# Optimization experiments

Hardware: AMD Instinct MI355X
Metric: run time of the kernel (lower is better)

Reference implementation:

```python
import jax, jax.numpy as jnp
import numpy as np

D_MODEL = 2048
N_HEADS = 16
HEAD_DIM = D_MODEL // N_HEADS  # 128
MAX_POS = 2048


def _precompute_cos_sin(max_pos, head_dim):
    inv_freq = 1.0 / (10000.0 ** (jnp.arange(0, head_dim, 2, dtype=jnp.float32) / head_dim))
    t = jnp.arange(max_pos, dtype=jnp.float32)
    freqs = jnp.outer(t, inv_freq)          # [max_pos, head_dim//2]
    emb = jnp.concatenate([freqs, freqs], axis=-1)  # [max_pos, head_dim]
    return jnp.cos(emb), jnp.sin(emb)


def _rotate_half(x):
    x1, x2 = x[..., : x.shape[-1] // 2], x[..., x.shape[-1] // 2 :]
    return jnp.concatenate([-x2, x1], axis=-1)


def setup_inputs() -> dict:
    key = jax.random.key(0)
    kx, kq, kk, kv, ko = jax.random.split(key, 5)
    B, S = 2, 2048
    x = jax.random.normal(kx, (B, S, D_MODEL), dtype=jnp.float32)
    scale = 1.0 / np.sqrt(D_MODEL)
    # torch Linear weights are [out_features, in_features]
    Wq = jax.random.normal(kq, (D_MODEL, D_MODEL), dtype=jnp.float32) * scale
    Wk = jax.random.normal(kk, (D_MODEL, D_MODEL), dtype=jnp.float32) * scale
    Wv = jax.random.normal(kv, (D_MODEL, D_MODEL), dtype=jnp.float32) * scale
    Wo = jax.random.normal(ko, (D_MODEL, D_MODEL), dtype=jnp.float32) * scale
    cos, sin = _precompute_cos_sin(MAX_POS, HEAD_DIM)
    # causal mask: True where attention is disallowed (masked_fill semantics)
    mask = jnp.triu(jnp.ones((S, S), dtype=bool), k=1)
    mask = jnp.broadcast_to(mask[None], (B, S, S))
    return {"x": x, "Wq": Wq, "Wk": Wk, "Wv": Wv, "Wo": Wo,
            "cos": cos, "sin": sin, "mask": mask}


def reference(x, Wq, Wk, Wv, Wo, cos, sin, mask):
    B, S, _ = x.shape
    H, Dh = N_HEADS, HEAD_DIM
    scaling = Dh ** -0.5

    def split_heads(y):  # [B,S,D] -> [B,H,S,Dh]
        return y.reshape(B, S, H, Dh).transpose(0, 2, 1, 3)

    q = split_heads(x @ Wq.T)
    k = split_heads(x @ Wk.T)
    v = split_heads(x @ Wv.T)

    c = cos[:S][None, None]  # [1,1,S,Dh]
    s = sin[:S][None, None]
    q = q * c + _rotate_half(q) * s
    k = k * c + _rotate_half(k) * s

    scores = jnp.einsum("bhqd,bhkd->bhqk", q, k) * scaling
    scores = jnp.where(mask[:, None], -jnp.inf, scores)
    attn = jax.nn.softmax(scores, axis=-1)
    out = jnp.einsum("bhqk,bhkd->bhqd", attn, v)  # [B,H,S,Dh]
    out = out.transpose(0, 2, 1, 3).reshape(B, S, H * Dh)
    return out @ Wo.T
```

## Files before the change

### kernel.cpp

```cpp
#include <hip/hip_runtime.h>

typedef float f32x4 __attribute__((ext_vector_type(4)));
typedef short s16x8 __attribute__((ext_vector_type(8)));
typedef unsigned short u16;
typedef u16 u16x4 __attribute__((ext_vector_type(4)));

#define SEQ 2048
#define BATCH 2
#define NH 16
#define DH 128
#define DM 2048
#define MROWS (BATCH * SEQ)

__device__ constexpr float SCALE2 = 0.12751879523531f;

__device__ __forceinline__ u16 f2bf(float f) {
  unsigned u = __float_as_uint(f);
  u += 0x7fffu + ((u >> 16) & 1u);
  return (u16)(u >> 16);
}
__device__ __forceinline__ float bf2f(u16 b) {
  return __uint_as_float(((unsigned)b) << 16);
}

__device__ __forceinline__ void gld_lds16(const void* g, void* l) {
  __builtin_amdgcn_global_load_lds(
      (const __attribute__((address_space(1))) unsigned int*)g,
      (__attribute__((address_space(3))) unsigned int*)l, 16, 0, 0);
}

__global__ __launch_bounds__(256) void cast_all(const float* __restrict__ x,
                                                const float* __restrict__ Wq,
                                                const float* __restrict__ Wk,
                                                const float* __restrict__ Wv,
                                                const float* __restrict__ Wo,
                                                u16* __restrict__ xb,
                                                u16* __restrict__ Wqkvb,
                                                u16* __restrict__ Wob) {
  long i = (long)blockIdx.x * 256 + threadIdx.x;
  const float* src;
  u16* dst;
  long off;
  if (i < 2097152)      { src = x;  dst = xb;              off = i; }
  else if (i < 3145728) { src = Wq; dst = Wqkvb;           off = i - 2097152; }
  else if (i < 4194304) { src = Wk; dst = Wqkvb + 4194304; off = i - 3145728; }
  else if (i < 5242880) { src = Wv; dst = Wqkvb + 8388608; off = i - 4194304; }
  else                  { src = Wo; dst = Wob;             off = i - 5242880; }
  float4 v = ((const float4*)src)[off];
  u16x4 o;
  o[0] = f2bf(v.x); o[1] = f2bf(v.y); o[2] = f2bf(v.z); o[3] = f2bf(v.w);
  ((u16x4*)dst)[off] = o;
}


#define BCOL(NF) (wn * 32 + ((NF) & 1) * 16 + ((NF) >> 1) * 64 + r)

#define GEMM_V3_BODY(A, B)                                                    \
  __shared__ u16 SMEM[49152];                                      \
  u16 (*Alds)[16384] = (u16(*)[16384])SMEM;                    \
  u16 (*Blds)[8192]  = (u16(*)[8192])(SMEM + 32768);           \
  const int tid = threadIdx.x, wave = tid >> 6, lane = tid & 63;              \
  const int r = lane & 15, g = lane >> 4;                                     \
  const int wm = wave >> 1, wn = wave & 1;                                    \
  const int bid = blockIdx.x;                                                 \
  const int swz = (bid & 7) * (gridDim.x >> 3) + (bid >> 3);                  \
  const int m0 = (swz & 15) * 256;                                            \
  const int n0 = (swz >> 4) * 128;                                            \
  const int lrow = lane >> 3;                                                 \
  const int csrc = (lane & 7) ^ lrow;                                         \
  f32x4 acc[4][4] = {};                                                       \
  s16x8 aF[2][4], bF[2][4];                                                   \
  STAGE_A(0, 0, 0); STAGE_B(0, 0, 0); STAGE_A(0, 1, 0); STAGE_B(0, 1, 0);     \
  STAGE_A(1, 0, 1); STAGE_B(1, 0, 1);                                         \
  asm volatile("s_waitcnt vmcnt(3)" ::: "memory");                            \
  __builtin_amdgcn_s_barrier();                                               \
  for (int t = 0; t < 32; ++t) {                                              \
    const int bt = t & 1, bn = bt ^ 1;                                        \
    const u16* Ab = Alds[bt];                                                 \
    const u16* Bb = Blds[bt];                                                 \
    READ_K(0);                                                                \
    __builtin_amdgcn_sched_barrier(0);                                        \
    READ_K(1);                                                                \
    if (t < 31) { STAGE_A(t + 1, 1, bn); STAGE_B(t + 1, 1, bn); }             \
    asm volatile("s_waitcnt lgkmcnt(8)" ::: "memory");                        \
    __builtin_amdgcn_sched_barrier(0);                                        \
    MFMA_K(0);                                                                \
    asm volatile("s_waitcnt lgkmcnt(0)" ::: "memory");                        \
    __builtin_amdgcn_sched_barrier(0);                                        \
    __builtin_amdgcn_s_barrier();                                             \
    if (t < 30) { STAGE_A(t + 2, 0, bt); STAGE_B(t + 2, 0, bt); }             \
    MFMA_K(1);                                                                \
    if (t < 30)       asm volatile("s_waitcnt vmcnt(3)" ::: "memory");        \
    else if (t == 30) asm volatile("s_waitcnt vmcnt(0)" ::: "memory");        \
    __builtin_amdgcn_s_barrier();                                             \
  }

#define STAGE_A(TA, MH, BUF) do {                                             \
  _Pragma("unroll") for (int i_ = 0; i_ < 2; ++i_) {                          \
    const int row0_ = (MH) * 128 + i_ * 64 + wave * 8;                        \
    gld_lds16(A + (long)(m0 + row0_ + lrow) * 2048 + (TA) * 64 + csrc * 8,    \
              &Alds[BUF][row0_ * 64]);                                        \
  } } while (0)
#define STAGE_B(TA, NHh, BUF) do {                                            \
    const int row0_ = (NHh) * 64 + wave * 8;                                  \
    gld_lds16(B + (long)(n0 + row0_ + lrow) * 2048 + (TA) * 64 + csrc * 8,    \
              &Blds[BUF][row0_ * 64]);                                        \
  } while (0)
#define READ_K(KK) do {                                                       \
  _Pragma("unroll") for (int mf = 0; mf < 4; ++mf) {                          \
    const int arow = wm * 64 + mf * 16 + r;                                   \
    aF[KK][mf] = *(const s16x8*)&Ab[arow * 64 +                               \
                                    ((((KK) * 4 + g) ^ (arow & 7)) * 8)];     \
  }                                                                           \
  _Pragma("unroll") for (int nf = 0; nf < 4; ++nf) {                          \
    const int brow = BCOL(nf);                                                \
    bF[KK][nf] = *(const s16x8*)&Bb[brow * 64 +                               \
                                    ((((KK) * 4 + g) ^ (brow & 7)) * 8)];     \
  } } while (0)
#define MFMA_K(KK) do {                                                       \
  __builtin_amdgcn_s_setprio(1);                                              \
  _Pragma("unroll") for (int mf = 0; mf < 4; ++mf)                            \
    _Pragma("unroll") for (int nf = 0; nf < 4; ++nf)                          \
      acc[mf][nf] = __builtin_amdgcn_mfma_f32_16x16x32_bf16(                  \
          aF[KK][mf], bF[KK][nf], acc[mf][nf], 0, 0, 0);                      \
  __builtin_amdgcn_s_setprio(0);                                              \
} while (0)

__global__ __launch_bounds__(512, 2) void gemm_qkv8(const u16* __restrict__ A,
                                                    const u16* __restrict__ B,
                                                    const float* __restrict__ cosT,
                                                    const float* __restrict__ sinT,
                                                    u16* __restrict__ Qo,
                                                    u16* __restrict__ Ko,
                                                    u16* __restrict__ Vt) {
  GEMM_V3_BODY(A, B)
  if (n0 < 4096) {
    u16* Cb = (n0 < 2048) ? Qo : Ko;
    const int nc0 = n0 & 2047;
#pragma unroll
    for (int mi = 0; mi < 4; ++mi)
#pragma unroll
      for (int nf = 0; nf < 2; ++nf) {
        const int dlo = wn * 32 + nf * 16 + r;
#pragma unroll
        for (int q = 0; q < 4; ++q) {
          const int row = m0 + wm * 64 + mi * 16 + g * 4 + q;
          const int spos = row & 2047;
          const float c = cosT[spos * 128 + dlo];
          const float s = sinT[spos * 128 + dlo];
          const float vlo = acc[mi][nf][q];
          const float vhi = acc[mi][nf + 2][q];
          Cb[(long)row * 2048 + nc0 + dlo]      = f2bf(vlo * c - vhi * s);
          Cb[(long)row * 2048 + nc0 + dlo + 64] = f2bf(vhi * c + vlo * s);
        }
      }
  } else {
    u16* T = SMEM;
#pragma unroll
    for (int mi = 0; mi < 4; ++mi)
#pragma unroll
      for (int ni = 0; ni < 4; ++ni) {
        const int d = BCOL(ni);
        const int sb = wm * 64 + mi * 16 + g * 4;
        u16x4 w;
#pragma unroll
        for (int q = 0; q < 4; ++q) w[q] = f2bf(acc[mi][ni][q]);
        *(u16x4*)&T[d * 256 + (((sb >> 3) ^ (d & 7)) << 3) + (sb & 7)] = w;
      }
    __syncthreads();
    const int b_ = m0 >> 11, s0l = m0 & 2047;
    const int hh = (n0 - 4096) >> 7;
    const int dd = tid >> 2, part = tid & 3;
    u16* vrow = Vt + ((long)((b_ * 16 + hh) * 128 + dd)) * 2048 + s0l;
#pragma unroll
    for (int cc = 0; cc < 8; ++cc) {
      const int chunk = cc * 4 + part;
      s16x8 v = *(const s16x8*)&T[dd * 256 + ((chunk ^ (dd & 7)) << 3)];
      *(s16x8*)&vrow[chunk * 8] = v;
    }
  }
}

__global__ __launch_bounds__(512, 2) void gemm_wo(const u16* __restrict__ A,
                                                  const u16* __restrict__ B,
                                                  float* __restrict__ C) {
  GEMM_V3_BODY(A, B)
#pragma unroll
  for (int mi = 0; mi < 4; ++mi)
#pragma unroll
    for (int ni = 0; ni < 4; ++ni) {
      const int col = n0 + BCOL(ni);
#pragma unroll
      for (int q = 0; q < 4; ++q)
        C[(long)(m0 + wm * 64 + mi * 16 + g * 4 + q) * 2048 + col] =
            acc[mi][ni][q];
    }
}

#undef MFMA_K
#undef READ_K
#undef STAGE_B
#undef STAGE_A
#undef GEMM_V3_BODY
#undef BCOL


__device__ __forceinline__ float softmax_swapped(
    f32x4 (&s)[4], float& mi, float& li,
    u16 (&pl)[16][64], int qbase, int k0, int r, int g) {
  const int q = qbase + r;
  const bool edge = (k0 + 63) > qbase;
  float v[16];
#pragma unroll
  for (int kk = 0; kk < 4; kk++)
#pragma unroll
    for (int i = 0; i < 4; i++) {
      float x = s[kk][i] * SCALE2;
      if (edge && (k0 + kk * 16 + g * 4 + i > q)) x = -1e30f;
      v[kk * 4 + i] = x;
    }
  float t8[8], t4[4];
#pragma unroll
  for (int j = 0; j < 8; j++) t8[j] = fmaxf(v[2 * j], v[2 * j + 1]);
#pragma unroll
  for (int j = 0; j < 4; j++) t4[j] = fmaxf(t8[2 * j], t8[2 * j + 1]);
  float mx = fmaxf(fmaxf(t4[0], t4[1]), fmaxf(t4[2], t4[3]));
  mx = fmaxf(mx, __shfl_xor(mx, 16, 64));
  mx = fmaxf(mx, __shfl_xor(mx, 32, 64));
  const float mnew = fmaxf(mi, mx);
  const float a = exp2f(mi - mnew);
  float p[16];
#pragma unroll
  for (int j = 0; j < 16; j++) p[j] = exp2f(v[j] - mnew);
  float s8[8], s4[4];
#pragma unroll
  for (int j = 0; j < 8; j++) s8[j] = p[2 * j] + p[2 * j + 1];
#pragma unroll
  for (int j = 0; j < 4; j++) s4[j] = s8[2 * j] + s8[2 * j + 1];
  float ps = (s4[0] + s4[1]) + (s4[2] + s4[3]);
  ps += __shfl_xor(ps, 16, 64);
  ps += __shfl_xor(ps, 32, 64);
  li = li * a + ps;
  mi = mnew;
  const int sw = (r & 7) << 3;
#pragma unroll
  for (int kk = 0; kk < 4; kk++) {
    u16x4 w;
#pragma unroll
    for (int i = 0; i < 4; i++) w[i] = f2bf(p[kk * 4 + i]);
    *(u16x4*)&pl[r][(kk * 16 + g * 4) ^ sw] = w;
  }
  return a;
}

__global__ __launch_bounds__(512, 4) void attn_kernel(const u16* __restrict__ Q,
                                                      const u16* __restrict__ K,
                                                      const u16* __restrict__ Vt,
                                                      u16* __restrict__ O) {
  __shared__ u16 Klds[2][64 * 128];
  __shared__ u16 Vlds[2][128 * 64];
  __shared__ u16 Plds[8][16][64];

  const int tid = threadIdx.x, wave = tid >> 6, lane = tid & 63;
  const int r = lane & 15, g = lane >> 4;
  const int bh = blockIdx.x & 31;
  const int jj = blockIdx.x >> 5;
  const int j = (jj < 8) ? jj : 23 - jj;
  const int h = bh & 15, b = bh >> 4;
  const bool isB = wave >= 4;
  const int w4 = wave & 3;
  const int strip = isB ? (31 - j) : j;
  const int q0 = strip * 64 + w4 * 16;
  const int nt = 32 - j;
  const int lastA = j;

  const u16* Qbh = Q + (long)b * SEQ * DM + h * DH;
  const u16* Kbh = K + (long)b * SEQ * DM + h * DH;
  const u16* Vbh = Vt + ((long)(b * NH + h)) * DH * SEQ;

  s16x8 qf[4];
#pragma unroll
  for (int jq = 0; jq < 4; jq++)
    qf[jq] = *(const s16x8*)&Qbh[(long)(q0 + r) * DM + jq * 32 + g * 8];

  f32x4 oacc[8] = {};
  float mi = -1e30f, li = 0.f;

#define STAGE_KV(KT, BU) do {                                                 \
  const int k0_ = (KT) * 64;                                                  \
  _Pragma("unroll") for (int c = 0; c < 2; ++c) {                             \
    const int s = c * 512 + tid;                                              \
    const int krow = s >> 4;                                                  \
    const int kch = (s & 15) ^ (krow & 7);                                    \
    gld_lds16(Kbh + (long)(k0_ + krow) * DM + kch * 8,                        \
              &Klds[BU][(c * 512 + wave * 64) * 8]);                          \
    const int vrow = s >> 3;                                                  \
    const int vch = (s & 7) ^ (vrow & 7);                                     \
    gld_lds16(Vbh + (long)vrow * SEQ + k0_ + vch * 8,                         \
              &Vlds[BU][(c * 512 + wave * 64) * 8]);                          \
  } } while (0)

  STAGE_KV(0, 0);
  __syncthreads();

  for (int kt = 0; kt < nt; ++kt) {
    const int bu = kt & 1;
    if (kt + 1 < nt) STAGE_KV(kt + 1, bu ^ 1);
    const int k0 = kt * 64;
    const u16* Kb = Klds[bu];
    const u16* Vb = Vlds[bu];

    const bool active = isB || (kt <= lastA);
    if (active) {
      f32x4 sacc[4] = {};
#pragma unroll
      for (int kk = 0; kk < 4; kk++) {
#pragma unroll
        for (int jq = 0; jq < 4; jq++) {
          s16x8 kf = *(const s16x8*)&Kb[(kk * 16 + r) * 128 +
                                        (((jq * 4 + g) ^ (r & 7)) * 8)];
          sacc[kk] = __builtin_amdgcn_mfma_f32_16x16x32_bf16(kf, qf[jq], sacc[kk], 0, 0, 0);
        }
      }
      float a = softmax_swapped(sacc, mi, li, Plds[wave], q0, k0, r, g);
      f32x4 av;
#pragma unroll
      for (int i = 0; i < 4; i++) av[i] = __shfl(a, g * 4 + i, 64);
#pragma unroll
      for (int f = 0; f < 8; f++)
#pragma unroll
        for (int i = 0; i < 4; i++) oacc[f][i] *= av[i];

      const int sw = (r & 7) << 3;
#pragma unroll
      for (int kc = 0; kc < 2; kc++) {
        s16x8 pf = *(const s16x8*)&Plds[wave][r][(kc * 32 + g * 8) ^ sw];
#pragma unroll
        for (int f = 0; f < 8; f++) {
          s16x8 vf = *(const s16x8*)&Vb[(f * 16 + r) * 64 +
                                        (((kc * 4 + g) ^ (r & 7)) * 8)];
          oacc[f] = __builtin_amdgcn_mfma_f32_16x16x32_bf16(pf, vf, oacc[f], 0, 0, 0);
        }
      }
    }
    __syncthreads();
  }
#undef STAGE_KV

  const float inv = 1.f / li;
  f32x4 iv;
#pragma unroll
  for (int i = 0; i < 4; i++) iv[i] = __shfl(inv, g * 4 + i, 64);
  u16* Obh = O + (long)b * SEQ * DM + h * DH;
#pragma unroll
  for (int f = 0; f < 8; f++)
#pragma unroll
    for (int i = 0; i < 4; i++)
      Obh[(long)(q0 + g * 4 + i) * DM + f * 16 + r] = f2bf(oacc[f][i] * iv[i]);
}

extern "C" void kernel_launch(void* const* d_in, const int* in_sizes, int n_in,
                              void* d_out, int out_size, void* d_ws, size_t ws_size,
                              hipStream_t stream) {
  const float* x    = (const float*)d_in[0];
  const float* Wq   = (const float*)d_in[1];
  const float* Wk   = (const float*)d_in[2];
  const float* Wv   = (const float*)d_in[3];
  const float* Wo   = (const float*)d_in[4];
  const float* cosT = (const float*)d_in[5];
  const float* sinT = (const float*)d_in[6];

  if (ws_size < (size_t)134217728) return;

  char* ws = (char*)d_ws;
  u16* xb    = (u16*)(ws);
  u16* Wqkvb = (u16*)(ws + 16777216);
  u16* Wob   = (u16*)(ws + 41943040);
  u16* Qlin  = (u16*)(ws + 50331648);
  u16* Klin  = (u16*)(ws + 67108864);
  u16* Vt    = (u16*)(ws + 100663296);
  u16* Olin  = (u16*)(ws + 117440512);

  cast_all<<<24576, 256, 0, stream>>>(x, Wq, Wk, Wv, Wo, xb, Wqkvb, Wob);

  gemm_qkv8<<<768, 512, 0, stream>>>(xb, Wqkvb, cosT, sinT, Qlin, Klin, Vt);

  attn_kernel<<<512, 512, 0, stream>>>(Qlin, Klin, Vt, Olin);

  gemm_wo<<<256, 512, 0, stream>>>(Olin, Wob, (float*)d_out);
}
```

Before: 247.7 us.

## Give each attention wave two query tiles and four strips per block

Measured after the change: 267.7 us. 1.08x slower.

```diff
diff --git a/kernel.cpp b/kernel.cpp
--- a/kernel.cpp
+++ b/kernel.cpp
@@ -253,38 +253,38 @@
   return a;
 }
 
-__global__ __launch_bounds__(512, 4) void attn_kernel(const u16* __restrict__ Q,
+__global__ __launch_bounds__(512, 2) void attn_kernel(const u16* __restrict__ Q,
                                                       const u16* __restrict__ K,
                                                       const u16* __restrict__ Vt,
                                                       u16* __restrict__ O) {
   __shared__ u16 Klds[2][64 * 128];
   __shared__ u16 Vlds[2][128 * 64];
-  __shared__ u16 Plds[8][16][64];
+  __shared__ u16 Plds[8][2][16][64];
 
   const int tid = threadIdx.x, wave = tid >> 6, lane = tid & 63;
   const int r = lane & 15, g = lane >> 4;
   const int bh = blockIdx.x & 31;
-  const int jj = blockIdx.x >> 5;
-  const int j = (jj < 8) ? jj : 23 - jj;
+  const int pg = blockIdx.x >> 5;
   const int h = bh & 15, b = bh >> 4;
-  const bool isB = wave >= 4;
-  const int w4 = wave & 3;
-  const int strip = isB ? (31 - j) : j;
-  const int q0 = strip * 64 + w4 * 16;
-  const int nt = 32 - j;
-  const int lastA = j;
+  const int sidx = wave >> 1;
+  const int strip = (sidx & 1) ? ((sidx & 2) ? 31 - pg : 15 - pg)
+                               : ((sidx & 2) ? 16 + pg : pg);
+  const int q0 = strip * 64 + (wave & 1) * 32;
+  const int nt = 32 - pg;
 
   const u16* Qbh = Q + (long)b * SEQ * DM + h * DH;
   const u16* Kbh = K + (long)b * SEQ * DM + h * DH;
   const u16* Vbh = Vt + ((long)(b * NH + h)) * DH * SEQ;
 
-  s16x8 qf[4];
-#pragma unroll
-  for (int jq = 0; jq < 4; jq++)
-    qf[jq] = *(const s16x8*)&Qbh[(long)(q0 + r) * DM + jq * 32 + g * 8];
-
-  f32x4 oacc[8] = {};
-  float mi = -1e30f, li = 0.f;
+  s16x8 qfA[4], qfB[4];
+#pragma unroll
+  for (int jq = 0; jq < 4; jq++) {
+    qfA[jq] = *(const s16x8*)&Qbh[(long)(q0 + r) * DM + jq * 32 + g * 8];
+    qfB[jq] = *(const s16x8*)&Qbh[(long)(q0 + 16 + r) * DM + jq * 32 + g * 8];
+  }
+
+  f32x4 oaccA[8] = {}, oaccB[8] = {};
+  float miA = -1e30f, liA = 0.f, miB = -1e30f, liB = 0.f;
 
 #define STAGE_KV(KT, BU) do {                                                 \
   const int k0_ = (KT) * 64;                                                  \
@@ -310,36 +310,45 @@
     const u16* Kb = Klds[bu];
     const u16* Vb = Vlds[bu];
 
-    const bool active = isB || (kt <= lastA);
-    if (active) {
-      f32x4 sacc[4] = {};
+    if (kt <= strip) {
+      f32x4 sA[4] = {}, sB[4] = {};
 #pragma unroll
       for (int kk = 0; kk < 4; kk++) {
 #pragma unroll
         for (int jq = 0; jq < 4; jq++) {
           s16x8 kf = *(const s16x8*)&Kb[(kk * 16 + r) * 128 +
                                         (((jq * 4 + g) ^ (r & 7)) * 8)];
-          sacc[kk] = __builtin_amdgcn_mfma_f32_16x16x32_bf16(kf, qf[jq], sacc[kk], 0, 0, 0);
+          sA[kk] = __builtin_amdgcn_mfma_f32_16x16x32_bf16(kf, qfA[jq], sA[kk], 0, 0, 0);
+          sB[kk] = __builtin_amdgcn_mfma_f32_16x16x32_bf16(kf, qfB[jq], sB[kk], 0, 0, 0);
         }
       }
-      float a = softmax_swapped(sacc, mi, li, Plds[wave], q0, k0, r, g);
-      f32x4 av;
-#pragma unroll
-      for (int i = 0; i < 4; i++) av[i] = __shfl(a, g * 4 + i, 64);
+      float aA = softmax_swapped(sA, miA, liA, Plds[wave][0], q0, k0, r, g);
+      float aB = softmax_swapped(sB, miB, liB, Plds[wave][1], q0 + 16, k0, r, g);
+      f32x4 avA, avB;
+#pragma unroll
+      for (int i = 0; i < 4; i++) {
+        avA[i] = __shfl(aA, g * 4 + i, 64);
+        avB[i] = __shfl(aB, g * 4 + i, 64);
+      }
 #pragma unroll
       for (int f = 0; f < 8; f++)
 #pragma unroll
-        for (int i = 0; i < 4; i++) oacc[f][i] *= av[i];
+        for (int i = 0; i < 4; i++) {
+          oaccA[f][i] *= avA[i];
+          oaccB[f][i] *= avB[i];
+        }
 
       const int sw = (r & 7) << 3;
 #pragma unroll
       for (int kc = 0; kc < 2; kc++) {
-        s16x8 pf = *(const s16x8*)&Plds[wave][r][(kc * 32 + g * 8) ^ sw];
+        s16x8 pfA = *(const s16x8*)&Plds[wave][0][r][(kc * 32 + g * 8) ^ sw];
+        s16x8 pfB = *(const s16x8*)&Plds[wave][1][r][(kc * 32 + g * 8) ^ sw];
 #pragma unroll
         for (int f = 0; f < 8; f++) {
           s16x8 vf = *(const s16x8*)&Vb[(f * 16 + r) * 64 +
                                         (((kc * 4 + g) ^ (r & 7)) * 8)];
-          oacc[f] = __builtin_amdgcn_mfma_f32_16x16x32_bf16(pf, vf, oacc[f], 0, 0, 0);
+          oaccA[f] = __builtin_amdgcn_mfma_f32_16x16x32_bf16(pfA, vf, oaccA[f], 0, 0, 0);
+          oaccB[f] = __builtin_amdgcn_mfma_f32_16x16x32_bf16(pfB, vf, oaccB[f], 0, 0, 0);
         }
       }
     }
@@ -347,16 +356,22 @@
   }
 #undef STAGE_KV
 
-  const float inv = 1.f / li;
-  f32x4 iv;
-#pragma unroll
-  for (int i = 0; i < 4; i++) iv[i] = __shfl(inv, g * 4 + i, 64);
+  const float invA = 1.f / liA;
+  const float invB = 1.f / liB;
+  f32x4 ivA, ivB;
+#pragma unroll
+  for (int i = 0; i < 4; i++) {
+    ivA[i] = __shfl(invA, g * 4 + i, 64);
+    ivB[i] = __shfl(invB, g * 4 + i, 64);
+  }
   u16* Obh = O + (long)b * SEQ * DM + h * DH;
 #pragma unroll
   for (int f = 0; f < 8; f++)
 #pragma unroll
-    for (int i = 0; i < 4; i++)
-      Obh[(long)(q0 + g * 4 + i) * DM + f * 16 + r] = f2bf(oacc[f][i] * iv[i]);
+    for (int i = 0; i < 4; i++) {
+      Obh[(long)(q0 + g * 4 + i) * DM + f * 16 + r] = f2bf(oaccA[f][i] * ivA[i]);
+      Obh[(long)(q0 + 16 + g * 4 + i) * DM + f * 16 + r] = f2bf(oaccB[f][i] * ivB[i]);
+    }
 }
 
 extern "C" void kernel_launch(void* const* d_in, const int* in_sizes, int n_in,
@@ -385,7 +400,7 @@
 
   gemm_qkv8<<<768, 512, 0, stream>>>(xb, Wqkvb, cosT, sinT, Qlin, Klin, Vt);
 
-  attn_kernel<<<512, 512, 0, stream>>>(Qlin, Klin, Vt, Olin);
+  attn_kernel<<<256, 512, 0, stream>>>(Qlin, Klin, Vt, Olin);
 
   gemm_wo<<<256, 512, 0, stream>>>(Olin, Wob, (float*)d_out);
 }
```

## Triple-buffer GEMM LDS tiles and double-buffer register fragments

Applied to the files above, without the earlier changes.

Result: slower. 362.9 us (+46.5%).

```diff
diff --git a/kernel.cpp b/kernel.cpp
--- a/kernel.cpp
+++ b/kernel.cpp
@@ -55,10 +55,62 @@
 
 #define BCOL(NF) (wn * 32 + ((NF) & 1) * 16 + ((NF) >> 1) * 64 + r)
 
-#define GEMM_V3_BODY(A, B)                                                    \
-  __shared__ u16 SMEM[49152];                                      \
-  u16 (*Alds)[16384] = (u16(*)[16384])SMEM;                    \
-  u16 (*Blds)[8192]  = (u16(*)[8192])(SMEM + 32768);           \
+#define STAGE6(TA, P) do {                                                    \
+  _Pragma("unroll") for (int m_ = 0; m_ < 4; ++m_) {                          \
+    const int row0_ = m_ * 64 + wave * 8;                                     \
+    gld_lds16(Amat + (long)(m0 + row0_ + lrow) * 2048 + (TA) * 64 + csrc * 8, \
+              &(P)[row0_ * 64]);                                              \
+  }                                                                           \
+  _Pragma("unroll") for (int n_ = 0; n_ < 2; ++n_) {                          \
+    const int row0_ = n_ * 64 + wave * 8;                                     \
+    gld_lds16(Bmat + (long)(n0 + row0_ + lrow) * 2048 + (TA) * 64 + csrc * 8, \
+              &(P)[16384 + row0_ * 64]);                                      \
+  } } while (0)
+
+#define READ_SET(KK, AF, BF, P) do {                                          \
+  _Pragma("unroll") for (int mf = 0; mf < 4; ++mf) {                          \
+    const int arow = wm * 64 + mf * 16 + r;                                   \
+    AF[KK][mf] = *(const s16x8*)&(P)[arow * 64 +                              \
+                                     ((((KK) * 4 + g) ^ (arow & 7)) * 8)];    \
+  }                                                                           \
+  _Pragma("unroll") for (int nf = 0; nf < 4; ++nf) {                          \
+    const int brow = BCOL(nf);                                                \
+    BF[KK][nf] = *(const s16x8*)&(P)[16384 + brow * 64 +                      \
+                                     ((((KK) * 4 + g) ^ (brow & 7)) * 8)];    \
+  } } while (0)
+
+#define MFMA_SET(KK, AF, BF) do {                                             \
+  __builtin_amdgcn_s_setprio(1);                                              \
+  _Pragma("unroll") for (int mf = 0; mf < 4; ++mf)                            \
+    _Pragma("unroll") for (int nf = 0; nf < 4; ++nf)                          \
+      acc[mf][nf] = __builtin_amdgcn_mfma_f32_16x16x32_bf16(                  \
+          AF[KK][mf], BF[KK][nf], acc[mf][nf], 0, 0, 0);                      \
+  __builtin_amdgcn_s_setprio(0);                                              \
+} while (0)
+
+#define TILE(T, AFC, BFC, AFN, BFN) do {                                      \
+  asm volatile("s_waitcnt lgkmcnt(8)" ::: "memory");                          \
+  __builtin_amdgcn_sched_barrier(0);                                          \
+  MFMA_SET(0, AFC, BFC);                                                      \
+  if ((T) < 30) STAGE6((T) + 2, pb2);                                         \
+  asm volatile("s_waitcnt lgkmcnt(0)" ::: "memory");                          \
+  __builtin_amdgcn_sched_barrier(0);                                          \
+  if ((T) < 30)       asm volatile("s_waitcnt vmcnt(6)" ::: "memory");        \
+  else if ((T) == 30) asm volatile("s_waitcnt vmcnt(0)" ::: "memory");        \
+  __builtin_amdgcn_s_barrier();                                               \
+  if ((T) < 31) {                                                             \
+    READ_SET(0, AFN, BFN, pb1);                                               \
+    __builtin_amdgcn_sched_barrier(0);                                        \
+    READ_SET(1, AFN, BFN, pb1);                                               \
+  }                                                                           \
+  MFMA_SET(1, AFC, BFC);                                                      \
+  { u16* tmp_ = pb0; pb0 = pb1; pb1 = pb2; pb2 = tmp_; }                      \
+} while (0)
+
+#define GEMM_V4_BODY(AIN, BIN)                                                \
+  __shared__ u16 SMEM[73728];                         \
+  const u16* Amat = (AIN);                                                    \
+  const u16* Bmat = (BIN);                                                    \
   const int tid = threadIdx.x, wave = tid >> 6, lane = tid & 63;              \
   const int r = lane & 15, g = lane >> 4;                                     \
   const int wm = wave >> 1, wn = wave & 1;                                    \
@@ -68,72 +120,29 @@
   const int n0 = (swz >> 4) * 128;                                            \
   const int lrow = lane >> 3;                                                 \
   const int csrc = (lane & 7) ^ lrow;                                         \
+  u16 *pb0 = SMEM, *pb1 = SMEM + 24576, *pb2 = SMEM + 49152;                  \
   f32x4 acc[4][4] = {};                                                       \
-  s16x8 aF[2][4], bF[2][4];                                                   \
-  STAGE_A(0, 0, 0); STAGE_B(0, 0, 0); STAGE_A(0, 1, 0); STAGE_B(0, 1, 0);     \
-  STAGE_A(1, 0, 1); STAGE_B(1, 0, 1);                                         \
-  asm volatile("s_waitcnt vmcnt(3)" ::: "memory");                            \
+  s16x8 aF0[2][4], bF0[2][4], aF1[2][4], bF1[2][4];                           \
+  STAGE6(0, pb0);                                                             \
+  STAGE6(1, pb1);                                                             \
+  asm volatile("s_waitcnt vmcnt(6)" ::: "memory");                            \
   __builtin_amdgcn_s_barrier();                                               \
-  for (int t = 0; t < 32; ++t) {                                              \
-    const int bt = t & 1, bn = bt ^ 1;                                        \
-    const u16* Ab = Alds[bt];                                                 \
-    const u16* Bb = Blds[bt];                                                 \
-    READ_K(0);                                                                \
-    __builtin_amdgcn_sched_barrier(0);                                        \
-    READ_K(1);                                                                \
-    if (t < 31) { STAGE_A(t + 1, 1, bn); STAGE_B(t + 1, 1, bn); }             \
-    asm volatile("s_waitcnt lgkmcnt(8)" ::: "memory");                        \
-    __builtin_amdgcn_sched_barrier(0);                                        \
-    MFMA_K(0);                                                                \
-    asm volatile("s_waitcnt lgkmcnt(0)" ::: "memory");                        \
-    __builtin_amdgcn_sched_barrier(0);                                        \
-    __builtin_amdgcn_s_barrier();                                             \
-    if (t < 30) { STAGE_A(t + 2, 0, bt); STAGE_B(t + 2, 0, bt); }             \
-    MFMA_K(1);                                                                \
-    if (t < 30)       asm volatile("s_waitcnt vmcnt(3)" ::: "memory");        \
-    else if (t == 30) asm volatile("s_waitcnt vmcnt(0)" ::: "memory");        \
-    __builtin_amdgcn_s_barrier();                                             \
+  READ_SET(0, aF0, bF0, pb0);                                                 \
+  __builtin_amdgcn_sched_barrier(0);                                          \
+  READ_SET(1, aF0, bF0, pb0);                                                 \
+  for (int t = 0; t < 32; t += 2) {                                           \
+    TILE(t,     aF0, bF0, aF1, bF1);                                          \
+    TILE(t + 1, aF1, bF1, aF0, bF0);                                          \
   }
 
-#define STAGE_A(TA, MH, BUF) do {                                             \
-  _Pragma("unroll") for (int i_ = 0; i_ < 2; ++i_) {                          \
-    const int row0_ = (MH) * 128 + i_ * 64 + wave * 8;                        \
-    gld_lds16(A + (long)(m0 + row0_ + lrow) * 2048 + (TA) * 64 + csrc * 8,    \
-              &Alds[BUF][row0_ * 64]);                                        \
-  } } while (0)
-#define STAGE_B(TA, NHh, BUF) do {                                            \
-    const int row0_ = (NHh) * 64 + wave * 8;                                  \
-    gld_lds16(B + (long)(n0 + row0_ + lrow) * 2048 + (TA) * 64 + csrc * 8,    \
-              &Blds[BUF][row0_ * 64]);                                        \
-  } while (0)
-#define READ_K(KK) do {                                                       \
-  _Pragma("unroll") for (int mf = 0; mf < 4; ++mf) {                          \
-    const int arow = wm * 64 + mf * 16 + r;                                   \
-    aF[KK][mf] = *(const s16x8*)&Ab[arow * 64 +                               \
-                                    ((((KK) * 4 + g) ^ (arow & 7)) * 8)];     \
-  }                                                                           \
-  _Pragma("unroll") for (int nf = 0; nf < 4; ++nf) {                          \
-    const int brow = BCOL(nf);                                                \
-    bF[KK][nf] = *(const s16x8*)&Bb[brow * 64 +                               \
-                                    ((((KK) * 4 + g) ^ (brow & 7)) * 8)];     \
-  } } while (0)
-#define MFMA_K(KK) do {                                                       \
-  __builtin_amdgcn_s_setprio(1);                                              \
-  _Pragma("unroll") for (int mf = 0; mf < 4; ++mf)                            \
-    _Pragma("unroll") for (int nf = 0; nf < 4; ++nf)                          \
-      acc[mf][nf] = __builtin_amdgcn_mfma_f32_16x16x32_bf16(                  \
-          aF[KK][mf], bF[KK][nf], acc[mf][nf], 0, 0, 0);                      \
-  __builtin_amdgcn_s_setprio(0);                                              \
-} while (0)
-
-__global__ __launch_bounds__(512, 2) void gemm_qkv8(const u16* __restrict__ A,
+__global__ __launch_bounds__(512, 1) void gemm_qkv8(const u16* __restrict__ A,
                                                     const u16* __restrict__ B,
                                                     const float* __restrict__ cosT,
                                                     const float* __restrict__ sinT,
                                                     u16* __restrict__ Qo,
                                                     u16* __restrict__ Ko,
                                                     u16* __restrict__ Vt) {
-  GEMM_V3_BODY(A, B)
+  GEMM_V4_BODY(A, B)
   if (n0 < 4096) {
     u16* Cb = (n0 < 2048) ? Qo : Ko;
     const int nc0 = n0 & 2047;
@@ -155,6 +164,7 @@
         }
       }
   } else {
+    __syncthreads();
     u16* T = SMEM;
 #pragma unroll
     for (int mi = 0; mi < 4; ++mi)
@@ -181,10 +191,10 @@
   }
 }
 
-__global__ __launch_bounds__(512, 2) void gemm_wo(const u16* __restrict__ A,
+__global__ __launch_bounds__(512, 1) void gemm_wo(const u16* __restrict__ A,
                                                   const u16* __restrict__ B,
                                                   float* __restrict__ C) {
-  GEMM_V3_BODY(A, B)
+  GEMM_V4_BODY(A, B)
 #pragma unroll
   for (int mi = 0; mi < 4; ++mi)
 #pragma unroll
@@ -197,11 +207,11 @@
     }
 }
 
-#undef MFMA_K
-#undef READ_K
-#undef STAGE_B
-#undef STAGE_A
-#undef GEMM_V3_BODY
+#undef GEMM_V4_BODY
+#undef TILE
+#undef MFMA_SET
+#undef READ_SET
+#undef STAGE6
 #undef BCOL
 
 
```
